# Performance work log

Hardware: AMD Instinct MI355X
Metric: run time of the kernel (lower is better)

## Reference

```python
import jax, jax.numpy as jnp
import numpy as np
from jax.scipy.linalg import expm

D_LOGIC = 128
D_MEM = 16
SO_DIM = D_MEM * (D_MEM - 1) // 2  # 120


def _linear_init(key, fan_in, shape):
    bound = 1.0 / np.sqrt(fan_in)
    return jax.random.uniform(key, shape, jnp.float32, -bound, bound)


def setup_inputs() -> dict:
    key = jax.random.key(0)
    ks = jax.random.split(key, 14)
    B, S = 4, 128
    return {
        "x_logic": jax.random.normal(ks[0], (B, S, D_LOGIC), jnp.float32),
        "x_memory": jax.random.normal(ks[1], (B, S, D_MEM), jnp.float32),
        # W_Q / W_K
        "Wq": _linear_init(ks[2], D_LOGIC, (D_LOGIC, D_LOGIC)),
        "bq": _linear_init(ks[3], D_LOGIC, (D_LOGIC,)),
        "Wk": _linear_init(ks[4], D_LOGIC, (D_LOGIC, D_LOGIC)),
        "bk": _linear_init(ks[5], D_LOGIC, (D_LOGIC,)),
        # gamma_net: Linear(d_logic, 2*d_logic) -> Tanh -> Linear(2*d_logic, so_dim)
        "W1": _linear_init(ks[6], D_LOGIC, (2 * D_LOGIC, D_LOGIC)),
        "b1": _linear_init(ks[7], D_LOGIC, (2 * D_LOGIC,)),
        "W2": _linear_init(ks[8], 2 * D_LOGIC, (SO_DIM, 2 * D_LOGIC)),
        "b2": _linear_init(ks[9], 2 * D_LOGIC, (SO_DIM,)),
        # out_proj: Linear(d_memory, d_memory)
        "Wo": _linear_init(ks[10], D_MEM, (D_MEM, D_MEM)),
        "bo": _linear_init(ks[11], D_MEM, (D_MEM,)),
    }


def reference(x_logic, x_memory, Wq, bq, Wk, bk, W1, b1, W2, b2, Wo, bo):
    B, S, d_logic = x_logic.shape
    dm = x_memory.shape[-1]

    # attention over logic stream
    Q = x_logic @ Wq.T + bq
    K = x_logic @ Wk.T + bk
    attn = jax.nn.softmax(
        jnp.einsum("bjd,bid->bji", Q, K) / jnp.sqrt(jnp.float32(d_logic)), axis=-1
    )  # [B, S(j), S(i)]

    # per-pair Lie-algebra params: delta[b,j,i] = x_logic[b,j] - x_logic[b,i]
    delta = x_logic[:, :, None, :] - x_logic[:, None, :, :]  # [B,S,S,d_logic]
    h = jnp.tanh(delta @ W1.T + b1)
    lie = h @ W2.T + b2  # [B,S,S,so_dim]

    # scatter into skew-symmetric matrices [B,S,S,dm,dm]
    r, c = np.triu_indices(dm, k=1)
    skew = jnp.zeros((B, S, S, dm, dm), x_logic.dtype)
    skew = skew.at[..., r, c].set(lie)
    skew = skew.at[..., c, r].set(-lie)

    # Lie-group exponential -> orthogonal transport matrices
    T_all = expm(skew)  # [B,S,S,dm,dm]

    # transported[b,j,i,:] = T[b,j,i] @ x_memory[b,i]
    transported = jnp.einsum("bjide,bie->bjid", T_all, x_memory)

    # attention-weighted aggregation over i
    settled = jnp.einsum("bji,bjid->bjd", attn, transported)  # [B,S,dm]

    out = settled @ Wo.T + bo
    return out, T_all
```

## Files before the change

kernel.cpp:

```cpp
#include <hip/hip_runtime.h>
#include <hip/hip_fp16.h>

#define S_LEN 128
#define DLOG  128
#define DMEM  16
#define SO    120
#define HDIM  256

typedef _Float16 v8h __attribute__((ext_vector_type(8)));
typedef __fp16 v2hf __attribute__((ext_vector_type(2)));
typedef float v4f __attribute__((ext_vector_type(4)));

union PkU { v2hf h; unsigned u; };
union V8U { v8h v; int u[4]; };

__device__ __forceinline__ v8h splat8(float x) {
  _Float16 h = (_Float16)x;
  v8h v = {h, h, h, h, h, h, h, h};
  return v;
}

__global__ __launch_bounds__(128) void qk_kernel(
    const float* __restrict__ xl, const float* __restrict__ Wq,
    const float* __restrict__ bq, const float* __restrict__ Wk,
    const float* __restrict__ bk, float* __restrict__ Q, float* __restrict__ K) {
  int bj = blockIdx.x, o = threadIdx.x;
  __shared__ float xs[128];
  xs[o] = xl[bj * 128 + o];
  __syncthreads();
  float aq = bq[o], ak = bk[o];
  const float* wq = Wq + o * 128;
  const float* wk = Wk + o * 128;
  #pragma unroll 4
  for (int d = 0; d < 128; ++d) {
    float x = xs[d];
    aq = fmaf(x, wq[d], aq);
    ak = fmaf(x, wk[d], ak);
  }
  Q[bj * 128 + o] = aq;
  K[bj * 128 + o] = ak;
}

__global__ __launch_bounds__(128) void attn_kernel(
    const float* __restrict__ Q, const float* __restrict__ K,
    float* __restrict__ attn) {
  int bj = blockIdx.x, b = bj >> 7, i = threadIdx.x;
  __shared__ float qs[128];
  __shared__ float red[128];
  qs[i] = Q[bj * 128 + i];
  __syncthreads();
  const float* kr = K + (b * 128 + i) * 128;
  float s = 0.f;
  #pragma unroll 4
  for (int d = 0; d < 128; ++d) s = fmaf(qs[d], kr[d], s);
  s *= 0.08838834764831845f;
  red[i] = s;
  __syncthreads();
  for (int off = 64; off; off >>= 1) {
    if (i < off) red[i] = fmaxf(red[i], red[i + off]);
    __syncthreads();
  }
  float m = red[0];
  __syncthreads();
  float e = expf(s - m);
  red[i] = e;
  __syncthreads();
  for (int off = 64; off; off >>= 1) {
    if (i < off) red[i] += red[i + off];
    __syncthreads();
  }
  attn[(size_t)bj * 128 + i] = e / red[0];
}

__global__ __launch_bounds__(256) void h_kernel(
    const float* __restrict__ xl, const float* __restrict__ W1,
    const float* __restrict__ b1, __half* __restrict__ hG) {
  __shared__ _Float16 w1s[128 * 136];
  __shared__ _Float16 dstage[64 * 136];
  __shared__ float xjs[128];
  int t = threadIdx.x;
  int blk = blockIdx.x;
  int bj = blk >> 1;
  int oh = blk & 1;
  int b = bj >> 7;
  int o0 = oh * 128;

  if (t < 128) xjs[t] = xl[bj * 128 + t];
  for (int idx = t; idx < 128 * 128; idx += 256) {
    int o = idx >> 7, k = idx & 127;
    w1s[o * 136 + k] = (_Float16)W1[(o0 + o) * 128 + k];
  }
  __syncthreads();

  int lane = t & 63, w = t >> 6;
  int nn = lane & 15, q = lane >> 4;
  int ow = o0 + w * 32;
  float bb0 = b1[ow + nn], bb1 = b1[ow + 16 + nn];
  const float* xb = xl + (size_t)b * 128 * 128;

  for (int pi = 0; pi < 2; ++pi) {
    for (int idx = t; idx < 64 * 128; idx += 256) {
      int i = idx >> 7, k = idx & 127;
      dstage[i * 136 + k] = (_Float16)(xjs[k] - xb[(pi * 64 + i) * 128 + k]);
    }
    __syncthreads();

    v4f acc[4][2];
    #pragma unroll
    for (int mi = 0; mi < 4; ++mi) {
      acc[mi][0] = (v4f){0.f, 0.f, 0.f, 0.f};
      acc[mi][1] = (v4f){0.f, 0.f, 0.f, 0.f};
    }
    #pragma unroll
    for (int ks = 0; ks < 4; ++ks) {
      v8h bf0 = *(const v8h*)&w1s[(w * 32 + nn) * 136 + ks * 32 + q * 8];
      v8h bf1 = *(const v8h*)&w1s[(w * 32 + 16 + nn) * 136 + ks * 32 + q * 8];
      #pragma unroll
      for (int mi = 0; mi < 4; ++mi) {
        v8h af = *(const v8h*)&dstage[(mi * 16 + nn) * 136 + ks * 32 + q * 8];
        acc[mi][0] = __builtin_amdgcn_mfma_f32_16x16x32_f16(af, bf0, acc[mi][0], 0, 0, 0);
        acc[mi][1] = __builtin_amdgcn_mfma_f32_16x16x32_f16(af, bf1, acc[mi][1], 0, 0, 0);
      }
    }
    #pragma unroll
    for (int mi = 0; mi < 4; ++mi) {
      #pragma unroll
      for (int nt = 0; nt < 2; ++nt) {
        int o = ow + nt * 16 + nn;
        float bbv = nt ? bb1 : bb0;
        #pragma unroll
        for (int reg = 0; reg < 4; ++reg) {
          int i = pi * 64 + mi * 16 + 4 * q + reg;
          float x = acc[mi][nt][reg] + bbv;
          float ax = fabsf(x);
          float e = __expf(-2.f * ax);
          float r = __fdividef(1.f - e, 1.f + e);
          r = copysignf(r, x);
          hG[(size_t)(bj * 128 + i) * 512 + o] = __float2half(r);
        }
      }
    }
    __syncthreads();
  }
}

__global__ __launch_bounds__(256) void lie_kernel(
    const float* __restrict__ W2g, const float* __restrict__ b2g,
    float* __restrict__ Tg) {
  __shared__ _Float16 w2t[128 * 136];
  int t = threadIdx.x, lane = t & 63;
  int wu = __builtin_amdgcn_readfirstlane(t >> 6);
  int pbase = blockIdx.x * 64 + wu * 16;
  int nn = lane & 15, q = lane >> 4;
  const _Float16* hf = (const _Float16*)Tg;

  v4f acc[8];
  #pragma unroll
  for (int tt = 0; tt < 8; ++tt) acc[tt] = (v4f){0.f, 0.f, 0.f, 0.f};

  const _Float16* hrow = hf + (size_t)(pbase + nn) * 512;
  for (int khalf = 0; khalf < 2; ++khalf) {
    __syncthreads();
    for (int idx = t; idx < 120 * 128; idx += 256) {
      int o = idx >> 7, kk = idx & 127;
      w2t[o * 136 + kk] = (_Float16)W2g[o * 256 + khalf * 128 + kk];
    }
    for (int idx = t; idx < 8 * 128; idx += 256)
      w2t[(120 + (idx >> 7)) * 136 + (idx & 127)] = (_Float16)0.f;
    __syncthreads();
    #pragma unroll
    for (int ks = 0; ks < 4; ++ks) {
      v8h ah = *(const v8h*)(hrow + khalf * 128 + ks * 32 + 8 * q);
      #pragma unroll
      for (int tt = 0; tt < 8; ++tt) {
        const v8h bf = *(const v8h*)(w2t + (16 * tt + nn) * 136 + ks * 32 + 8 * q);
        acc[tt] = __builtin_amdgcn_mfma_f32_16x16x32_f16(ah, bf, acc[tt], 0, 0, 0);
      }
    }
  }

  _Float16* hw = (_Float16*)Tg;
  #pragma unroll
  for (int tt = 0; tt < 8; ++tt) {
    int n16 = 16 * tt + nn;
    if (n16 < 120) {
      float bb = b2g[n16];
      #pragma unroll
      for (int reg = 0; reg < 4; ++reg) {
        size_t p = (size_t)(pbase + 4 * q + reg);
        hw[p * 512 + 256 + n16] = (_Float16)(acc[tt][reg] + bb);
      }
    }
  }
}

__device__ __forceinline__ void split8(const float* x, v8h& hi, v8h& lo) {
  union U { v8h v; v2hf p[4]; } H, L;
  #pragma unroll
  for (int i = 0; i < 4; ++i) {
    float a = x[2 * i], b = x[2 * i + 1];
    v2hf h = __builtin_amdgcn_cvt_pkrtz(a, b);
    float ra = (float)h[0], rb = (float)h[1];
    v2hf l = __builtin_amdgcn_cvt_pkrtz(a - ra, b - rb);
    H.p[i] = h;
    L.p[i] = l;
  }
  hi = H.v;
  lo = L.v;
}

__device__ __forceinline__ int lie_idx(int rr, int cc) {
  return 15 * rr - ((rr * (rr - 1)) >> 1) + cc - rr - 1;
}

__global__ __launch_bounds__(256) void expm_kernel(
    float* __restrict__ Tg, const float* __restrict__ attn,
    const float* __restrict__ xm, float* __restrict__ part) {
  __shared__ char lds[12288] __attribute__((aligned(16)));
  __shared__ float sred[4][16];
  int t = threadIdx.x, lane = t & 63;
  int wu = __builtin_amdgcn_readfirstlane(t >> 6);
  int pbase = blockIdx.x * 8 + wu * 2;
  int nn = lane & 15, q = lane >> 4, b8 = (q & 1) * 8;
  char* wb = lds + wu * 3072;
  _Float16* lieS = (_Float16*)wb;
  float* ErB = (float*)(wb + 512);
  const _Float16* hf = (const _Float16*)Tg;

  int idxA = ((2 * (q & 1)) * 16 + nn) * 4;
  int idxB = idxA + 64;

  float scv[2];
  int sv[2];
  #pragma unroll
  for (int j = 0; j < 2; ++j) {
    size_t p = (size_t)(pbase + j);
    _Float16 a0 = (lane < 120) ? hf[p * 512 + 256 + lane] : (_Float16)0.f;
    _Float16 a1 = (lane < 56) ? hf[p * 512 + 320 + lane] : (_Float16)0.f;
    lieS[j * 128 + lane] = a0;
    lieS[j * 128 + 64 + lane] = a1;
    float f0 = (float)a0, f1 = (float)a1;
    float s2 = f0 * f0 + f1 * f1;
    #pragma unroll
    for (int off = 1; off < 64; off <<= 1) s2 += __shfl_xor(s2, off, 64);
    float bound = sqrtf(s2);
    int s = 0;
    while (bound > 1.0f && s < 12) { bound *= 0.5f; s++; }
    sv[j] = __builtin_amdgcn_readfirstlane(s);
    scv[j] = ldexpf(1.0f, -s);
  }
  asm volatile("s_waitcnt lgkmcnt(0)" ::: "memory");

  V8U Apk[2], BfA[2];
  v4f Af[2];
  #pragma unroll
  for (int j = 0; j < 2; ++j) {
    const _Float16* lp = lieS + j * 128;
    float sc = scv[j];
    float av[8];
    #pragma unroll
    for (int jj = 0; jj < 8; ++jj) {
      int c = b8 + jj;
      int rr = min(nn, c), c2 = max(nn, c);
      float lv = (c == nn) ? 0.f : (float)lp[lie_idx(rr, c2)];
      av[jj] = (c == nn) ? 0.f : ((c > nn) ? lv : -lv) * sc;
    }
    #pragma unroll
    for (int i = 0; i < 4; ++i) {
      PkU u;
      u.h = __builtin_amdgcn_cvt_pkrtz(av[2 * i], av[2 * i + 1]);
      Apk[j].u[i] = (int)u.u;
      BfA[j].u[i] = Apk[j].u[i] ^ 0x80008000;
    }
    #pragma unroll
    for (int reg = 0; reg < 4; ++reg) {
      int r = 4 * q + reg;
      int rr = min(r, nn), c2 = max(r, nn);
      float lv = (r == nn) ? 0.f : (float)lp[lie_idx(rr, c2)];
      Af[j][reg] = (r == nn) ? 0.f : ((nn > r) ? lv : -lv) * sc;
    }
  }

  V8U IC1, IC2;
  #pragma unroll
  for (int i = 0; i < 4; ++i) {
    float d0 = (b8 + 2 * i == nn) ? 1.f : 0.f;
    float d1 = (b8 + 2 * i + 1 == nn) ? 1.f : 0.f;
    PkU u1, u2;
    u1.h = __builtin_amdgcn_cvt_pkrtz(10.666667f * d0, 10.666667f * d1);
    u2.h = __builtin_amdgcn_cvt_pkrtz(2.1333333f * d0, 2.1333333f * d1);
    IC1.u[i] = (int)u1.u;
    IC2.u[i] = (int)u2.u;
  }

  v4f z4 = {0.f, 0.f, 0.f, 0.f};

  v4f cB[2];
  #pragma unroll
  for (int j = 0; j < 2; ++j)
    cB[j] = __builtin_amdgcn_mfma_f32_16x16x32_f16(Apk[j].v, BfA[j].v, z4, 0, 0, 0);

  V8U fB[2];
  #pragma unroll
  for (int j = 0; j < 2; ++j) {
    PkU u0, u1;
    u0.h = __builtin_amdgcn_cvt_pkrtz(cB[j][0], cB[j][1]);
    u1.h = __builtin_amdgcn_cvt_pkrtz(cB[j][2], cB[j][3]);
    fB[j].u[0] = __builtin_amdgcn_ds_bpermute(idxA, (int)u0.u);
    fB[j].u[1] = __builtin_amdgcn_ds_bpermute(idxA, (int)u1.u);
    fB[j].u[2] = __builtin_amdgcn_ds_bpermute(idxB, (int)u0.u);
    fB[j].u[3] = __builtin_amdgcn_ds_bpermute(idxB, (int)u1.u);
  }

  v4f cB2[2];
  #pragma unroll
  for (int j = 0; j < 2; ++j)
    cB2[j] = __builtin_amdgcn_mfma_f32_16x16x32_f16(fB[j].v, fB[j].v, z4, 0, 0, 0);

  V8U fB2[2];
  #pragma unroll
  for (int j = 0; j < 2; ++j) {
    PkU u0, u1;
    u0.h = __builtin_amdgcn_cvt_pkrtz(cB2[j][0], cB2[j][1]);
    u1.h = __builtin_amdgcn_cvt_pkrtz(cB2[j][2], cB2[j][3]);
    fB2[j].u[0] = __builtin_amdgcn_ds_bpermute(idxA, (int)u0.u);
    fB2[j].u[1] = __builtin_amdgcn_ds_bpermute(idxA, (int)u1.u);
    fB2[j].u[2] = __builtin_amdgcn_ds_bpermute(idxB, (int)u0.u);
    fB2[j].u[3] = __builtin_amdgcn_ds_bpermute(idxB, (int)u1.u);
  }

  v8h k1a = splat8(7.9365079e-4f);
  v8h k1b = splat8(0.17777778f);
  v8h k2a = splat8(8.8183422e-5f);
  v8h k2b = splat8(2.5396825e-2f);
  V8U M1[2], M2[2];
  #pragma unroll
  for (int j = 0; j < 2; ++j) {
    M1[j].v = fB2[j].v * k1a + (fB[j].v * k1b + IC1.v);
    M2[j].v = fB2[j].v * k2a + (fB[j].v * k2b + IC2.v);
  }

  v4f Cc[2], Qc[2];
  #pragma unroll
  for (int j = 0; j < 2; ++j) {
    v4f c3m = __builtin_amdgcn_mfma_f32_16x16x32_f16(M1[j].v, fB2[j].v, z4, 0, 0, 0);
    v4f c4m = __builtin_amdgcn_mfma_f32_16x16x32_f16(M2[j].v, fB2[j].v, z4, 0, 0, 0);
    #pragma unroll
    for (int reg = 0; reg < 4; ++reg) {
      float dg = (4 * q + reg == nn) ? 1.f : 0.f;
      Cc[j][reg] = fmaf(c3m[reg], 2.44140625e-4f,
                        fmaf(cB[j][reg], 0.25f, dg + Af[j][reg]));
      Qc[j][reg] = fmaf(c4m[reg], 2.44140625e-4f, cB[j][reg] * 0.083333333f);
    }
  }

  V8U fQ[2];
  #pragma unroll
  for (int j = 0; j < 2; ++j) {
    PkU u0, u1;
    u0.h = __builtin_amdgcn_cvt_pkrtz(Qc[j][0], Qc[j][1]);
    u1.h = __builtin_amdgcn_cvt_pkrtz(Qc[j][2], Qc[j][3]);
    fQ[j].u[0] = __builtin_amdgcn_ds_bpermute(idxA, (int)u0.u);
    fQ[j].u[1] = __builtin_amdgcn_ds_bpermute(idxA, (int)u1.u);
    fQ[j].u[2] = __builtin_amdgcn_ds_bpermute(idxB, (int)u0.u);
    fQ[j].u[3] = __builtin_amdgcn_ds_bpermute(idxB, (int)u1.u);
  }

  v4f E[2];
  #pragma unroll
  for (int j = 0; j < 2; ++j) {
    v4f c5 = __builtin_amdgcn_mfma_f32_16x16x32_f16(Apk[j].v, fQ[j].v, z4, 0, 0, 0);
    E[j] = Cc[j] + c5 * 0.5f;
  }

  int smax = max(sv[0], sv[1]);
  for (int it = 0; it < smax; ++it) {
    #pragma unroll
    for (int j = 0; j < 2; ++j) {
      if (it < sv[j]) {
        float* Erp = ErB + j * 320;
        PkU u0, u1;
        u0.h = __builtin_amdgcn_cvt_pkrtz(E[j][0], E[j][1]);
        u1.h = __builtin_amdgcn_cvt_pkrtz(E[j][2], E[j][3]);
        V8U bfe;
        bfe.u[0] = __builtin_amdgcn_ds_bpermute(idxA, (int)u0.u);
        bfe.u[1] = __builtin_amdgcn_ds_bpermute(idxA, (int)u1.u);
        bfe.u[2] = __builtin_amdgcn_ds_bpermute(idxB, (int)u0.u);
        bfe.u[3] = __builtin_amdgcn_ds_bpermute(idxB, (int)u1.u);
        #pragma unroll
        for (int reg = 0; reg < 4; ++reg)
          Erp[(4 * q + reg) * 20 + nn] = E[j][reg];
        asm volatile("s_waitcnt lgkmcnt(0)" ::: "memory");
        float4 a0 = *(const float4*)(Erp + nn * 20 + b8);
        float4 a1 = *(const float4*)(Erp + nn * 20 + b8 + 4);
        float xa[8] = {a0.x, a0.y, a0.z, a0.w, a1.x, a1.y, a1.z, a1.w};
        v8h ahi, alo;
        split8(xa, ahi, alo);
        v8h Ecat = (q < 2) ? ahi : alo;
        v4f z = {0.f, 0.f, 0.f, 0.f};
        E[j] = __builtin_amdgcn_mfma_f32_16x16x32_f16(Ecat, bfe.v, z, 0, 0, 0);
      }
    }
  }

  float pacc[4] = {0.f, 0.f, 0.f, 0.f};
  #pragma unroll
  for (int j = 0; j < 2; ++j) {
    int p = pbase + j;
    float* dst = Tg + (size_t)p * 256;
    #pragma unroll
    for (int reg = 0; reg < 4; ++reg)
      dst[(4 * q + reg) * 16 + nn] = E[j][reg];
    int b = p >> 14, i = p & 127;
    float xv = xm[((b << 7) + i) * 16 + nn];
    float aw = attn[(size_t)p] * xv;
    #pragma unroll
    for (int reg = 0; reg < 4; ++reg)
      pacc[reg] = fmaf(aw, E[j][reg], pacc[reg]);
  }
  #pragma unroll
  for (int reg = 0; reg < 4; ++reg) {
    #pragma unroll
    for (int off = 1; off < 16; off <<= 1)
      pacc[reg] += __shfl_xor(pacc[reg], off, 64);
  }
  if (nn == 0) {
    #pragma unroll
    for (int reg = 0; reg < 4; ++reg) sred[wu][4 * q + reg] = pacc[reg];
  }
  __syncthreads();
  if (t < 16)
    part[(size_t)blockIdx.x * 16 + t] =
        sred[0][t] + sred[1][t] + sred[2][t] + sred[3][t];
}

__global__ __launch_bounds__(64) void settle_fin_kernel(
    const float* __restrict__ part, const float* __restrict__ Wo,
    const float* __restrict__ bo, float* __restrict__ outp) {
  int bj = blockIdx.x, t = threadIdx.x;
  int r = t & 15, e0 = t >> 4;
  const float* pb = part + (size_t)bj * 256;
  float s = pb[e0 * 16 + r] + pb[(e0 + 4) * 16 + r] +
            pb[(e0 + 8) * 16 + r] + pb[(e0 + 12) * 16 + r];
  __shared__ float sf[64];
  sf[t] = s;
  __syncthreads();
  if (t < 16) sf[t] = sf[t] + sf[16 + t] + sf[32 + t] + sf[48 + t];
  __syncthreads();
  if (t < 16) {
    float o = bo[t];
    const float* wr = Wo + t * 16;
    #pragma unroll
    for (int c = 0; c < 16; ++c) o = fmaf(wr[c], sf[c], o);
    outp[bj * 16 + t] = o;
  }
}

extern "C" void kernel_launch(void* const* d_in, const int* in_sizes, int n_in,
                              void* d_out, int out_size, void* d_ws,
                              size_t ws_size, hipStream_t stream) {
  const float* xl = (const float*)d_in[0];
  const float* xm = (const float*)d_in[1];
  const float* Wq = (const float*)d_in[2];
  const float* bq = (const float*)d_in[3];
  const float* Wk = (const float*)d_in[4];
  const float* bk = (const float*)d_in[5];
  const float* W1 = (const float*)d_in[6];
  const float* b1 = (const float*)d_in[7];
  const float* W2 = (const float*)d_in[8];
  const float* b2 = (const float*)d_in[9];
  const float* Wo = (const float*)d_in[10];
  const float* bo = (const float*)d_in[11];
  float* outp = (float*)d_out;
  float* Tg = outp + 8192;
  float* wsf = (float*)d_ws;
  float* Q = wsf;
  float* K = wsf + 65536;
  float* attn = wsf + 131072;
  float* part = wsf + 196608;

  hipLaunchKernelGGL(qk_kernel, dim3(512), dim3(128), 0, stream, xl, Wq, bq, Wk, bk, Q, K);
  hipLaunchKernelGGL(attn_kernel, dim3(512), dim3(128), 0, stream, Q, K, attn);
  hipLaunchKernelGGL(h_kernel, dim3(1024), dim3(256), 0, stream, xl, W1, b1, (__half*)Tg);
  hipLaunchKernelGGL(lie_kernel, dim3(1024), dim3(256), 0, stream, W2, b2, Tg);
  hipLaunchKernelGGL(expm_kernel, dim3(8192), dim3(256), 0, stream, Tg, attn, xm, part);
  hipLaunchKernelGGL(settle_fin_kernel, dim3(512), dim3(64), 0, stream, part, Wo, bo, outp);
}
```

Measured before the change: 206.6 us.

## Factor delta@W1 as per-row projection difference and fuse tanh into lie kernel

Uses linearity: (x_j - x_i)W1^T = u_j - u_i, where u = x W1^T is computed once per row inside the Q/K projection kernel. The pairwise GEMM in h_kernel is removed; lie_kernel now builds tanh(u_j - u_i + b1) in shared memory and feeds it to the W2 MFMA, so the fp16 hidden activations no longer round-trip through global memory. The workspace buffer u aliases part, which is only written later by expm, and the larger fused projection kernel adds some per-block work.

After: 238.2 us. +15.3%, slower.

```diff
diff --git a/kernel.cpp b/kernel.cpp
--- a/kernel.cpp
+++ b/kernel.cpp
@@ -20,25 +20,30 @@
   return v;
 }
 
-__global__ __launch_bounds__(128) void qk_kernel(
+__global__ __launch_bounds__(512) void qku_kernel(
     const float* __restrict__ xl, const float* __restrict__ Wq,
     const float* __restrict__ bq, const float* __restrict__ Wk,
-    const float* __restrict__ bk, float* __restrict__ Q, float* __restrict__ K) {
-  int bj = blockIdx.x, o = threadIdx.x;
+    const float* __restrict__ bk, const float* __restrict__ W1,
+    float* __restrict__ Q, float* __restrict__ K, float* __restrict__ u) {
+  int bj = blockIdx.x, t = threadIdx.x;
   __shared__ float xs[128];
-  xs[o] = xl[bj * 128 + o];
-  __syncthreads();
-  float aq = bq[o], ak = bk[o];
-  const float* wq = Wq + o * 128;
-  const float* wk = Wk + o * 128;
+  if (t < 128) xs[t] = xl[bj * 128 + t];
+  __syncthreads();
+  const float* wr;
+  float acc;
+  int o;
+  if (t < 128) {
+    o = t; wr = Wq + o * 128; acc = bq[o];
+  } else if (t < 256) {
+    o = t - 128; wr = Wk + o * 128; acc = bk[o];
+  } else {
+    o = t - 256; wr = W1 + o * 128; acc = 0.f;
+  }
   #pragma unroll 4
-  for (int d = 0; d < 128; ++d) {
-    float x = xs[d];
-    aq = fmaf(x, wq[d], aq);
-    ak = fmaf(x, wk[d], ak);
-  }
-  Q[bj * 128 + o] = aq;
-  K[bj * 128 + o] = ak;
+  for (int d = 0; d < 128; ++d) acc = fmaf(xs[d], wr[d], acc);
+  if (t < 128) Q[bj * 128 + o] = acc;
+  else if (t < 256) K[bj * 128 + o] = acc;
+  else u[bj * 256 + o] = acc;
 }
 
 __global__ __launch_bounds__(128) void attn_kernel(
@@ -72,93 +77,27 @@
   attn[(size_t)bj * 128 + i] = e / red[0];
 }
 
-__global__ __launch_bounds__(256) void h_kernel(
-    const float* __restrict__ xl, const float* __restrict__ W1,
-    const float* __restrict__ b1, __half* __restrict__ hG) {
-  __shared__ _Float16 w1s[128 * 136];
-  __shared__ _Float16 dstage[64 * 136];
-  __shared__ float xjs[128];
-  int t = threadIdx.x;
+__global__ __launch_bounds__(256) void lie_kernel(
+    const float* __restrict__ W2g, const float* __restrict__ b2g,
+    const float* __restrict__ ug, const float* __restrict__ b1g,
+    float* __restrict__ Tg) {
+  __shared__ _Float16 w2t[128 * 136];
+  __shared__ _Float16 ht[64 * 136];
+  __shared__ float b1s[128];
+  __shared__ float ujs[128];
+  int t = threadIdx.x, lane = t & 63;
+  int wu = __builtin_amdgcn_readfirstlane(t >> 6);
   int blk = blockIdx.x;
   int bj = blk >> 1;
-  int oh = blk & 1;
+  int i0 = (blk & 1) << 6;
   int b = bj >> 7;
-  int o0 = oh * 128;
-
-  if (t < 128) xjs[t] = xl[bj * 128 + t];
-  for (int idx = t; idx < 128 * 128; idx += 256) {
-    int o = idx >> 7, k = idx & 127;
-    w1s[o * 136 + k] = (_Float16)W1[(o0 + o) * 128 + k];
-  }
-  __syncthreads();
-
-  int lane = t & 63, w = t >> 6;
+  int pbase = blk * 64 + wu * 16;
   int nn = lane & 15, q = lane >> 4;
-  int ow = o0 + w * 32;
-  float bb0 = b1[ow + nn], bb1 = b1[ow + 16 + nn];
-  const float* xb = xl + (size_t)b * 128 * 128;
-
-  for (int pi = 0; pi < 2; ++pi) {
-    for (int idx = t; idx < 64 * 128; idx += 256) {
-      int i = idx >> 7, k = idx & 127;
-      dstage[i * 136 + k] = (_Float16)(xjs[k] - xb[(pi * 64 + i) * 128 + k]);
-    }
-    __syncthreads();
-
-    v4f acc[4][2];
-    #pragma unroll
-    for (int mi = 0; mi < 4; ++mi) {
-      acc[mi][0] = (v4f){0.f, 0.f, 0.f, 0.f};
-      acc[mi][1] = (v4f){0.f, 0.f, 0.f, 0.f};
-    }
-    #pragma unroll
-    for (int ks = 0; ks < 4; ++ks) {
-      v8h bf0 = *(const v8h*)&w1s[(w * 32 + nn) * 136 + ks * 32 + q * 8];
-      v8h bf1 = *(const v8h*)&w1s[(w * 32 + 16 + nn) * 136 + ks * 32 + q * 8];
-      #pragma unroll
-      for (int mi = 0; mi < 4; ++mi) {
-        v8h af = *(const v8h*)&dstage[(mi * 16 + nn) * 136 + ks * 32 + q * 8];
-        acc[mi][0] = __builtin_amdgcn_mfma_f32_16x16x32_f16(af, bf0, acc[mi][0], 0, 0, 0);
-        acc[mi][1] = __builtin_amdgcn_mfma_f32_16x16x32_f16(af, bf1, acc[mi][1], 0, 0, 0);
-      }
-    }
-    #pragma unroll
-    for (int mi = 0; mi < 4; ++mi) {
-      #pragma unroll
-      for (int nt = 0; nt < 2; ++nt) {
-        int o = ow + nt * 16 + nn;
-        float bbv = nt ? bb1 : bb0;
-        #pragma unroll
-        for (int reg = 0; reg < 4; ++reg) {
-          int i = pi * 64 + mi * 16 + 4 * q + reg;
-          float x = acc[mi][nt][reg] + bbv;
-          float ax = fabsf(x);
-          float e = __expf(-2.f * ax);
-          float r = __fdividef(1.f - e, 1.f + e);
-          r = copysignf(r, x);
-          hG[(size_t)(bj * 128 + i) * 512 + o] = __float2half(r);
-        }
-      }
-    }
-    __syncthreads();
-  }
-}
-
-__global__ __launch_bounds__(256) void lie_kernel(
-    const float* __restrict__ W2g, const float* __restrict__ b2g,
-    float* __restrict__ Tg) {
-  __shared__ _Float16 w2t[128 * 136];
-  int t = threadIdx.x, lane = t & 63;
-  int wu = __builtin_amdgcn_readfirstlane(t >> 6);
-  int pbase = blockIdx.x * 64 + wu * 16;
-  int nn = lane & 15, q = lane >> 4;
-  const _Float16* hf = (const _Float16*)Tg;
 
   v4f acc[8];
   #pragma unroll
   for (int tt = 0; tt < 8; ++tt) acc[tt] = (v4f){0.f, 0.f, 0.f, 0.f};
 
-  const _Float16* hrow = hf + (size_t)(pbase + nn) * 512;
   for (int khalf = 0; khalf < 2; ++khalf) {
     __syncthreads();
     for (int idx = t; idx < 120 * 128; idx += 256) {
@@ -167,10 +106,22 @@
     }
     for (int idx = t; idx < 8 * 128; idx += 256)
       w2t[(120 + (idx >> 7)) * 136 + (idx & 127)] = (_Float16)0.f;
+    if (t < 128) b1s[t] = b1g[khalf * 128 + t];
+    else ujs[t - 128] = ug[bj * 256 + khalf * 128 + (t - 128)];
     __syncthreads();
+    for (int idx = t; idx < 64 * 128; idx += 256) {
+      int i = idx >> 7, kk = idx & 127;
+      float x = ujs[kk] + b1s[kk] -
+                ug[(size_t)(b * 128 + i0 + i) * 256 + khalf * 128 + kk];
+      float ax = fabsf(x);
+      float e = __expf(-2.f * ax);
+      float r = __fdividef(1.f - e, 1.f + e);
+      ht[i * 136 + kk] = (_Float16)copysignf(r, x);
+    }
+    __syncthreads();
     #pragma unroll
     for (int ks = 0; ks < 4; ++ks) {
-      v8h ah = *(const v8h*)(hrow + khalf * 128 + ks * 32 + 8 * q);
+      v8h ah = *(const v8h*)&ht[(wu * 16 + nn) * 136 + ks * 32 + 8 * q];
       #pragma unroll
       for (int tt = 0; tt < 8; ++tt) {
         const v8h bf = *(const v8h*)(w2t + (16 * tt + nn) * 136 + ks * 32 + 8 * q);
@@ -477,12 +428,12 @@
   float* Q = wsf;
   float* K = wsf + 65536;
   float* attn = wsf + 131072;
+  float* u = wsf + 196608;
   float* part = wsf + 196608;
 
-  hipLaunchKernelGGL(qk_kernel, dim3(512), dim3(128), 0, stream, xl, Wq, bq, Wk, bk, Q, K);
+  hipLaunchKernelGGL(qku_kernel, dim3(512), dim3(512), 0, stream, xl, Wq, bq, Wk, bk, W1, Q, K, u);
   hipLaunchKernelGGL(attn_kernel, dim3(512), dim3(128), 0, stream, Q, K, attn);
-  hipLaunchKernelGGL(h_kernel, dim3(1024), dim3(256), 0, stream, xl, W1, b1, (__half*)Tg);
-  hipLaunchKernelGGL(lie_kernel, dim3(1024), dim3(256), 0, stream, W2, b2, Tg);
+  hipLaunchKernelGGL(lie_kernel, dim3(1024), dim3(256), 0, stream, W2, b2, u, b1, Tg);
   hipLaunchKernelGGL(expm_kernel, dim3(8192), dim3(256), 0, stream, Tg, attn, xm, part);
   hipLaunchKernelGGL(settle_fin_kernel, dim3(512), dim3(64), 0, stream, part, Wo, bo, outp);
 }
```
